# Optimization experiments

Measured on AMD Instinct MI355X. Metric: run time of the kernel, lower is better.

Reference implementation:

```python
import jax, jax.numpy as jnp
import numpy as np

B, D, C = 16384, 2048, 1000  # batch, in_features (feature dim), out_features (classes)
INIT_SCALE = 10.0
EPS = 1e-12


def setup_inputs() -> dict:
    key = jax.random.key(0)
    k1, k2 = jax.random.split(key)
    x = jax.random.normal(k1, (B, D), dtype=jnp.float32)
    weights = jax.random.normal(k2, (C, D), dtype=jnp.float32)  # prototypes
    scales = jnp.ones((1,), dtype=jnp.float32) * INIT_SCALE
    return {"x": x, "weights": weights, "scales": scales}


def reference(x, weights, scales):
    # Pairwise Euclidean distance between features [B,D] and prototypes [C,D]
    x2 = jnp.sum(x * x, axis=-1, keepdims=True)            # [B,1]
    w2 = jnp.sum(weights * weights, axis=-1)               # [C]
    cross = jnp.einsum('bd,cd->bc', x, weights)            # [B,C]
    d2 = jnp.maximum(x2 + w2[None, :] - 2.0 * cross, EPS)  # clamp for sqrt stability
    distances = jnp.sqrt(d2)                               # [B,C]
    logits = -scales * distances  # dml forward: -self.learn(distances)
    return logits
```

## Files before the change

kernel.cpp:

```cpp
#include <hip/hip_runtime.h>
#include <hip/hip_bf16.h>
#include <stdint.h>

#define B_ROWS 16384
#define D_K    2048
#define C_COLS 1000
#define C_PAD  1024
#define EPS_D2 1e-12f

typedef __attribute__((ext_vector_type(8))) short bf16x8;
typedef __attribute__((ext_vector_type(4))) float f32x4;

__device__ __forceinline__ void async16(void* lds, const void* g) {
    __builtin_amdgcn_global_load_lds(
        (const __attribute__((address_space(1))) unsigned int*)g,
        (__attribute__((address_space(3))) unsigned int*)lds,
        16, 0, 0);
}

__device__ __forceinline__ uint2 pack_bf16x4(float4 v) {
    union { __hip_bfloat162 h; uint32_t u; } a, b;
    a.h = __float22bfloat162_rn(make_float2(v.x, v.y));
    b.h = __float22bfloat162_rn(make_float2(v.z, v.w));
    uint2 r; r.x = a.u; r.y = b.u; return r;
}

__global__ __launch_bounds__(256) void prep_all(
    const float* __restrict__ x, const float* __restrict__ w,
    __hip_bfloat16* __restrict__ xb, __hip_bfloat16* __restrict__ wb,
    float* __restrict__ x2, float* __restrict__ w2) {
    const int t = threadIdx.x;
    const int wave = t >> 6;
    const int lane = t & 63;
    const int row = blockIdx.x * 4 + wave;

    const float* src;
    uint4* dst;
    float* norm_out;
    bool valid;
    if (row < B_ROWS) {
        src = x + (size_t)row * D_K;
        dst = (uint4*)(xb + (size_t)row * D_K);
        norm_out = x2 + row;
        valid = true;
    } else {
        int c = row - B_ROWS;
        src = w + (size_t)c * D_K;
        dst = (uint4*)(wb + (size_t)c * D_K);
        norm_out = w2 + c;
        valid = (c < C_COLS);
    }

    float4 v[8];
    if (valid) {
        const float4* s4 = (const float4*)src;
        #pragma unroll
        for (int i = 0; i < 4; i++) {
            v[2 * i]     = s4[2 * lane + 128 * i];
            v[2 * i + 1] = s4[2 * lane + 1 + 128 * i];
        }
    } else {
        #pragma unroll
        for (int i = 0; i < 8; i++) v[i] = make_float4(0.f, 0.f, 0.f, 0.f);
    }

    float ss = 0.f;
    #pragma unroll
    for (int i = 0; i < 8; i++)
        ss += v[i].x * v[i].x + v[i].y * v[i].y + v[i].z * v[i].z + v[i].w * v[i].w;

    #pragma unroll
    for (int i = 0; i < 4; i++) {
        uint2 a = pack_bf16x4(v[2 * i]);
        uint2 b = pack_bf16x4(v[2 * i + 1]);
        uint4 p; p.x = a.x; p.y = a.y; p.z = b.x; p.w = b.y;
        dst[lane + 64 * i] = p;
    }

    #pragma unroll
    for (int off = 32; off > 0; off >>= 1) ss += __shfl_down(ss, off, 64);
    if (lane == 0 && valid) *norm_out = ss;
}

__global__ __launch_bounds__(256) void dml_gemm(
    const __hip_bfloat16* __restrict__ A,
    const __hip_bfloat16* __restrict__ Bm,
    const float* __restrict__ x2, const float* __restrict__ w2,
    const float* __restrict__ scales, float* __restrict__ out)
{
    __shared__ __align__(16) char smem[32 * 132 * 4];
    __hip_bfloat16* lsA = (__hip_bfloat16*)smem;
    __hip_bfloat16* lsB = (__hip_bfloat16*)(smem + 8192);
    float* lsC = (float*)smem;

    const int tid  = threadIdx.x;
    const int wave = tid >> 6;
    const int lane = tid & 63;

    const int id  = blockIdx.y * 8 + blockIdx.x;
    const int xcd = id & 7;
    const int j   = id >> 3;
    const int m0  = (xcd * 16 + (j >> 3)) * 128;
    const int n0  = (j & 7) * 128;

    const int wm = wave >> 1;
    const int wn = wave & 1;

    const int srow = wave * 32 + (lane >> 2);
    const int slot = lane & 3;
    const int scol = (slot ^ ((srow >> 1) & 3)) * 8;
    const __hip_bfloat16* gA0 = A  + (size_t)(m0 + srow) * D_K + scol;
    const __hip_bfloat16* gA1 = gA0 + (size_t)16 * D_K;
    const __hip_bfloat16* gB0 = Bm + (size_t)(n0 + srow) * D_K + scol;
    const __hip_bfloat16* gB1 = gB0 + (size_t)16 * D_K;
    char* lA0 = (char*)lsA + wave * 32 * 64 + lane * 16;
    char* lA1 = lA0 + 16 * 64;
    char* lB0 = (char*)lsB + wave * 32 * 64 + lane * 16;
    char* lB1 = lB0 + 16 * 64;

    const int fr  = lane & 15;
    const int fq  = lane >> 4;
    const int fsw = (fr >> 1) & 3;
    const __hip_bfloat16* fA = lsA + (wm * 64 + fr) * 32 + (fq ^ fsw) * 8;
    const __hip_bfloat16* fB = lsB + (wn * 64 + fr) * 32 + (fq ^ fsw) * 8;

    f32x4 acc[4][4] = {};

    for (int k0 = 0; k0 < D_K; k0 += 32) {
        __syncthreads();
        async16(lA0, gA0); async16(lA1, gA1);
        async16(lB0, gB0); async16(lB1, gB1);
        gA0 += 32; gA1 += 32; gB0 += 32; gB1 += 32;
        __syncthreads();

        bf16x8 a[4], b[4];
        #pragma unroll
        for (int i = 0; i < 4; i++) a[i] = *(const bf16x8*)(fA + i * 16 * 32);
        #pragma unroll
        for (int j2 = 0; j2 < 4; j2++) b[j2] = *(const bf16x8*)(fB + j2 * 16 * 32);
        #pragma unroll
        for (int i = 0; i < 4; i++)
            #pragma unroll
            for (int j2 = 0; j2 < 4; j2++)
                acc[i][j2] = __builtin_amdgcn_mfma_f32_16x16x32_bf16(a[i], b[j2], acc[i][j2], 0, 0, 0);
    }

    const float s = scales[0];
    const int colb  = wn * 64 + fr;
    const int rowlb = wm * 64 + fq * 4;

    float w2v[4];
    #pragma unroll
    for (int j2 = 0; j2 < 4; j2++) w2v[j2] = w2[n0 + colb + j2 * 16];
    float x2v[4][4];
    #pragma unroll
    for (int i = 0; i < 4; i++)
        #pragma unroll
        for (int r = 0; r < 4; r++) x2v[i][r] = x2[m0 + rowlb + i * 16 + r];

    __syncthreads();

    const int rr  = tid >> 3;
    const int gmb = m0 + (rr & 15) + (rr >> 4) * 64;
    #pragma unroll
    for (int i = 0; i < 4; i++) {
        #pragma unroll
        for (int j2 = 0; j2 < 4; j2++)
            #pragma unroll
            for (int r = 0; r < 4; r++) {
                float d2 = x2v[i][r] + w2v[j2] - 2.0f * acc[i][j2][r];
                d2 = fmaxf(d2, EPS_D2);
                lsC[(wm * 16 + fq * 4 + r) * 132 + colb + j2 * 16] = -s * __builtin_sqrtf(d2);
            }
        __syncthreads();
        {
            float* orow = out + (size_t)(gmb + i * 16) * C_COLS + n0;
            #pragma unroll
            for (int q = 0; q < 4; q++) {
                const int f = (tid & 7) + 8 * q;
                if ((n0 >> 2) + f < C_COLS / 4) {
                    float4 val = *(const float4*)(lsC + rr * 132 + f * 4);
                    *(float4*)(orow + f * 4) = val;
                }
            }
        }
        __syncthreads();
    }
}

extern "C" void kernel_launch(void* const* d_in, const int* in_sizes, int n_in,
                              void* d_out, int out_size, void* d_ws, size_t ws_size,
                              hipStream_t stream) {
    const float* x      = (const float*)d_in[0];
    const float* w      = (const float*)d_in[1];
    const float* scales = (const float*)d_in[2];
    float* out = (float*)d_out;

    char* ws = (char*)d_ws;
    __hip_bfloat16* xb = (__hip_bfloat16*)ws;
    __hip_bfloat16* wb = (__hip_bfloat16*)(ws + (size_t)B_ROWS * D_K * 2);
    float* x2 = (float*)(ws + (size_t)B_ROWS * D_K * 2 + (size_t)C_PAD * D_K * 2);
    float* w2 = x2 + B_ROWS;

    prep_all<<<dim3((B_ROWS + C_PAD) / 4), dim3(256), 0, stream>>>(x, w, xb, wb, x2, w2);
    dml_gemm<<<dim3(8, B_ROWS / 128), dim3(256), 0, stream>>>(xb, wb, x2, w2, scales, out);
}
```

Baseline: 309.7 us.

## Use 256x256 tiles with 4-stage async LDS pipeline in distance GEMM

Grows the GEMM tile from 128x128 to 256x256 with 512 threads and a 4-buffer ring of asynchronous global-to-LDS loads. Next-tile loads are interleaved with MFMA groups, and there is one barrier per K step instead of two. The LDS-staged epilogue becomes direct global stores. The intent is to hide load latency, raise arithmetic intensity and cut barrier overhead. In exchange it uses 128KB of LDS and more accumulators per thread, which may limit occupancy, and the direct stores are less coalesced.

```diff
diff --git a/kernel.cpp b/kernel.cpp
--- a/kernel.cpp
+++ b/kernel.cpp
@@ -7,6 +7,13 @@
 #define C_COLS 1000
 #define C_PAD  1024
 #define EPS_D2 1e-12f
+
+#define BM 256
+#define BN 256
+#define BK 32
+#define NT (D_K / BK)
+#define BUF_BYTES 32768
+#define NBUF 4
 
 typedef __attribute__((ext_vector_type(8))) short bf16x8;
 typedef __attribute__((ext_vector_type(4))) float f32x4;
@@ -82,109 +89,130 @@
     if (lane == 0 && valid) *norm_out = ss;
 }
 
-__global__ __launch_bounds__(256) void dml_gemm(
+__global__ __launch_bounds__(512, 2) void dml_gemm(
     const __hip_bfloat16* __restrict__ A,
     const __hip_bfloat16* __restrict__ Bm,
     const float* __restrict__ x2, const float* __restrict__ w2,
     const float* __restrict__ scales, float* __restrict__ out)
 {
-    __shared__ __align__(16) char smem[32 * 132 * 4];
-    __hip_bfloat16* lsA = (__hip_bfloat16*)smem;
-    __hip_bfloat16* lsB = (__hip_bfloat16*)(smem + 8192);
-    float* lsC = (float*)smem;
+    __shared__ __align__(16) char smem[NBUF * BUF_BYTES];
 
     const int tid  = threadIdx.x;
     const int wave = tid >> 6;
     const int lane = tid & 63;
-
-    const int id  = blockIdx.y * 8 + blockIdx.x;
+    const int wm = wave >> 2;
+    const int wn = wave & 3;
+
+    const int id  = blockIdx.x;
     const int xcd = id & 7;
-    const int j   = id >> 3;
-    const int m0  = (xcd * 16 + (j >> 3)) * 128;
-    const int n0  = (j & 7) * 128;
-
-    const int wm = wave >> 1;
-    const int wn = wave & 1;
-
-    const int srow = wave * 32 + (lane >> 2);
-    const int slot = lane & 3;
-    const int scol = (slot ^ ((srow >> 1) & 3)) * 8;
-    const __hip_bfloat16* gA0 = A  + (size_t)(m0 + srow) * D_K + scol;
-    const __hip_bfloat16* gA1 = gA0 + (size_t)16 * D_K;
-    const __hip_bfloat16* gB0 = Bm + (size_t)(n0 + srow) * D_K + scol;
-    const __hip_bfloat16* gB1 = gB0 + (size_t)16 * D_K;
-    char* lA0 = (char*)lsA + wave * 32 * 64 + lane * 16;
-    char* lA1 = lA0 + 16 * 64;
-    char* lB0 = (char*)lsB + wave * 32 * 64 + lane * 16;
-    char* lB1 = lB0 + 16 * 64;
-
-    const int fr  = lane & 15;
-    const int fq  = lane >> 4;
-    const int fsw = (fr >> 1) & 3;
-    const __hip_bfloat16* fA = lsA + (wm * 64 + fr) * 32 + (fq ^ fsw) * 8;
-    const __hip_bfloat16* fB = lsB + (wn * 64 + fr) * 32 + (fq ^ fsw) * 8;
-
-    f32x4 acc[4][4] = {};
-
-    for (int k0 = 0; k0 < D_K; k0 += 32) {
-        __syncthreads();
-        async16(lA0, gA0); async16(lA1, gA1);
-        async16(lB0, gB0); async16(lB1, gB1);
-        gA0 += 32; gA1 += 32; gB0 += 32; gB1 += 32;
-        __syncthreads();
-
-        bf16x8 a[4], b[4];
-        #pragma unroll
-        for (int i = 0; i < 4; i++) a[i] = *(const bf16x8*)(fA + i * 16 * 32);
-        #pragma unroll
-        for (int j2 = 0; j2 < 4; j2++) b[j2] = *(const bf16x8*)(fB + j2 * 16 * 32);
-        #pragma unroll
-        for (int i = 0; i < 4; i++)
+    const int j5  = id >> 3;
+    const int m0  = (xcd * 8 + (j5 & 7)) * BM;
+    const int n0  = (j5 >> 3) * BN;
+
+    const int L0 = tid, L1 = tid + 512;
+    const int r0 = L0 >> 2, g0 = (L0 & 3) ^ ((r0 >> 1) & 3);
+    const int r1 = L1 >> 2, g1 = (L1 & 3) ^ ((r1 >> 1) & 3);
+    const __hip_bfloat16* pA0 = A  + (size_t)(m0 + r0) * D_K + g0 * 8;
+    const __hip_bfloat16* pA1 = A  + (size_t)(m0 + r1) * D_K + g1 * 8;
+    const __hip_bfloat16* pB0 = Bm + (size_t)(n0 + r0) * D_K + g0 * 8;
+    const __hip_bfloat16* pB1 = Bm + (size_t)(n0 + r1) * D_K + g1 * 8;
+    char* ldA0 = smem + L0 * 16;
+    char* ldA1 = smem + L1 * 16;
+    char* ldB0 = smem + 16384 + L0 * 16;
+    char* ldB1 = smem + 16384 + L1 * 16;
+
+    const int fr = lane & 15;
+    const int fq = lane >> 4;
+    const int ksw = (fq ^ ((fr >> 1) & 3)) * 16;
+    const char* fA = smem + (wm * 128 + fr) * 64 + ksw;
+    const char* fB = smem + 16384 + (wn * 64 + fr) * 64 + ksw;
+
+    f32x4 acc[8][4] = {};
+
+    #pragma unroll
+    for (int tgt = 0; tgt < 3; ++tgt) {
+        const int sbo = tgt * BUF_BYTES;
+        async16(ldA0 + sbo, pA0 + tgt * BK);
+        async16(ldA1 + sbo, pA1 + tgt * BK);
+        async16(ldB0 + sbo, pB0 + tgt * BK);
+        async16(ldB1 + sbo, pB1 + tgt * BK);
+    }
+    asm volatile("s_waitcnt vmcnt(8)" ::: "memory");
+    __builtin_amdgcn_s_barrier();
+    __builtin_amdgcn_sched_barrier(0);
+
+    #pragma unroll 1
+    for (int t = 0; t < NT; ++t) {
+        const int bo  = (t & 3) * BUF_BYTES;
+        const int tgt = t + 3;
+        const bool do_stage = (tgt < NT);
+        const int sbo = (tgt & 3) * BUF_BYTES;
+
+        if (do_stage) {
+            async16(ldA0 + sbo, pA0 + tgt * BK);
+            async16(ldA1 + sbo, pA1 + tgt * BK);
+        }
+        bf16x8 b[4], a[4];
+        #pragma unroll
+        for (int q = 0; q < 4; ++q) b[q] = *(const bf16x8*)(fB + bo + q * 1024);
+        #pragma unroll
+        for (int i = 0; i < 4; ++i) a[i] = *(const bf16x8*)(fA + bo + i * 1024);
+        __builtin_amdgcn_s_setprio(1);
+        #pragma unroll
+        for (int i = 0; i < 4; ++i)
             #pragma unroll
-            for (int j2 = 0; j2 < 4; j2++)
-                acc[i][j2] = __builtin_amdgcn_mfma_f32_16x16x32_bf16(a[i], b[j2], acc[i][j2], 0, 0, 0);
+            for (int q = 0; q < 4; ++q)
+                acc[i][q] = __builtin_amdgcn_mfma_f32_16x16x32_bf16(a[i], b[q], acc[i][q], 0, 0, 0);
+        __builtin_amdgcn_s_setprio(0);
+
+        if (do_stage) {
+            async16(ldB0 + sbo, pB0 + tgt * BK);
+            async16(ldB1 + sbo, pB1 + tgt * BK);
+        }
+        #pragma unroll
+        for (int i = 0; i < 4; ++i) a[i] = *(const bf16x8*)(fA + bo + (4 + i) * 1024);
+        __builtin_amdgcn_s_setprio(1);
+        #pragma unroll
+        for (int i = 0; i < 4; ++i)
+            #pragma unroll
+            for (int q = 0; q < 4; ++q)
+                acc[4 + i][q] = __builtin_amdgcn_mfma_f32_16x16x32_bf16(a[i], b[q], acc[4 + i][q], 0, 0, 0);
+        __builtin_amdgcn_s_setprio(0);
+
+        if (t < NT - 3)      asm volatile("s_waitcnt vmcnt(8)" ::: "memory");
+        else if (t == NT - 3) asm volatile("s_waitcnt vmcnt(4)" ::: "memory");
+        else if (t == NT - 2) asm volatile("s_waitcnt vmcnt(0)" ::: "memory");
+        if (t < NT - 1) {
+            __builtin_amdgcn_s_barrier();
+            __builtin_amdgcn_sched_barrier(0);
+        }
     }
 
     const float s = scales[0];
-    const int colb  = wn * 64 + fr;
-    const int rowlb = wm * 64 + fq * 4;
+    const int colb = n0 + wn * 64 + fr;
+    const int rowb = m0 + wm * 128 + fq * 4;
 
     float w2v[4];
     #pragma unroll
-    for (int j2 = 0; j2 < 4; j2++) w2v[j2] = w2[n0 + colb + j2 * 16];
-    float x2v[4][4];
-    #pragma unroll
-    for (int i = 0; i < 4; i++)
-        #pragma unroll
-        for (int r = 0; r < 4; r++) x2v[i][r] = x2[m0 + rowlb + i * 16 + r];
-
-    __syncthreads();
-
-    const int rr  = tid >> 3;
-    const int gmb = m0 + (rr & 15) + (rr >> 4) * 64;
-    #pragma unroll
-    for (int i = 0; i < 4; i++) {
-        #pragma unroll
-        for (int j2 = 0; j2 < 4; j2++)
-            #pragma unroll
-            for (int r = 0; r < 4; r++) {
-                float d2 = x2v[i][r] + w2v[j2] - 2.0f * acc[i][j2][r];
-                d2 = fmaxf(d2, EPS_D2);
-                lsC[(wm * 16 + fq * 4 + r) * 132 + colb + j2 * 16] = -s * __builtin_sqrtf(d2);
-            }
-        __syncthreads();
-        {
-            float* orow = out + (size_t)(gmb + i * 16) * C_COLS + n0;
-            #pragma unroll
-            for (int q = 0; q < 4; q++) {
-                const int f = (tid & 7) + 8 * q;
-                if ((n0 >> 2) + f < C_COLS / 4) {
-                    float4 val = *(const float4*)(lsC + rr * 132 + f * 4);
-                    *(float4*)(orow + f * 4) = val;
+    for (int q = 0; q < 4; ++q) w2v[q] = w2[colb + q * 16];
+
+    #pragma unroll
+    for (int i = 0; i < 8; ++i) {
+        float x2v[4];
+        #pragma unroll
+        for (int r = 0; r < 4; ++r) x2v[r] = x2[rowb + i * 16 + r];
+        #pragma unroll
+        for (int q = 0; q < 4; ++q) {
+            if (colb + q * 16 < C_COLS) {
+                float* orow = out + (size_t)(rowb + i * 16) * C_COLS + colb + q * 16;
+                #pragma unroll
+                for (int r = 0; r < 4; ++r) {
+                    float d2 = x2v[r] + w2v[q] - 2.0f * acc[i][q][r];
+                    d2 = fmaxf(d2, EPS_D2);
+                    orow[(size_t)r * C_COLS] = -s * __builtin_sqrtf(d2);
                 }
             }
         }
-        __syncthreads();
     }
 }
 
@@ -203,5 +231,5 @@
     float* w2 = x2 + B_ROWS;
 
     prep_all<<<dim3((B_ROWS + C_PAD) / 4), dim3(256), 0, stream>>>(x, w, xb, wb, x2, w2);
-    dml_gemm<<<dim3(8, B_ROWS / 128), dim3(256), 0, stream>>>(xb, wb, x2, w2, scales, out);
-}
+    dml_gemm<<<dim3((B_ROWS / BM) * (C_PAD / BN)), dim3(512), 0, stream>>>(xb, wb, x2, w2, scales, out);
+}
```

After: 286.7 us. 1.08x faster.
